# Performance work log

Hardware: AMD Instinct MI355X
Metric: run time of the kernel (lower is better)

## Reference

```python
import jax, jax.numpy as jnp
import numpy as np

DIM = 512
HEADS = 8
HEAD_DIM = DIM // HEADS
MLP_HIDDEN = int(DIM * 4.0)
B, N = 4, 2048
LS_INIT = 1e-5
EPS = 1e-5


def _layernorm(x, w, b):
    mu = jnp.mean(x, axis=-1, keepdims=True)
    var = jnp.mean(jnp.square(x - mu), axis=-1, keepdims=True)
    return (x - mu) * jax.lax.rsqrt(var + EPS) * w + b


def setup_inputs() -> dict:
    key = jax.random.key(0)
    ks = jax.random.split(key, 12)
    s = 0.02
    return {
        "x": jax.random.normal(ks[0], (B, N, DIM), jnp.float32),
        "rel_pos_bias": jax.random.normal(ks[1], (HEADS, N, N), jnp.float32),
        "qkv_w": jax.random.normal(ks[2], (DIM, 3 * DIM), jnp.float32) * s,
        "qkv_b": jnp.zeros((3 * DIM,), jnp.float32),
        "out_w": jax.random.normal(ks[3], (DIM, DIM), jnp.float32) * s,
        "out_b": jnp.zeros((DIM,), jnp.float32),
        "ln1_w": jnp.ones((DIM,), jnp.float32),
        "ln1_b": jnp.zeros((DIM,), jnp.float32),
        "ln2_w": jnp.ones((DIM,), jnp.float32),
        "ln2_b": jnp.zeros((DIM,), jnp.float32),
        "ffn_w1": jax.random.normal(ks[4], (DIM, MLP_HIDDEN), jnp.float32) * s,
        "ffn_b1": jnp.zeros((MLP_HIDDEN,), jnp.float32),
        "ffn_w2": jax.random.normal(ks[5], (MLP_HIDDEN, DIM), jnp.float32) * s,
        "ffn_b2": jnp.zeros((DIM,), jnp.float32),
        "gamma1": jnp.full((DIM,), LS_INIT, jnp.float32),
        "gamma2": jnp.full((DIM,), LS_INIT, jnp.float32),
    }


def reference(x, rel_pos_bias, qkv_w, qkv_b, out_w, out_b, ln1_w, ln1_b,
              ln2_w, ln2_b, ffn_w1, ffn_b1, ffn_w2, ffn_b2, gamma1, gamma2):
    # Pre-norm MHA with relative-position bias
    y = _layernorm(x, ln1_w, ln1_b)                       # [B,N,C]
    qkv = y @ qkv_w + qkv_b                               # [B,N,3C]
    qkv = qkv.reshape(B, N, 3, HEADS, HEAD_DIM)
    q = jnp.transpose(qkv[:, :, 0], (0, 2, 1, 3))         # [B,H,N,D]
    k = jnp.transpose(qkv[:, :, 1], (0, 2, 1, 3))
    v = jnp.transpose(qkv[:, :, 2], (0, 2, 1, 3))
    scale = 1.0 / np.sqrt(HEAD_DIM).astype(np.float32)
    attn = jnp.einsum("bhid,bhjd->bhij", q, k) * scale    # [B,H,N,N]
    attn = attn + rel_pos_bias[None]
    attn = jax.nn.softmax(attn, axis=-1)
    out = jnp.einsum("bhij,bhjd->bhid", attn, v)          # [B,H,N,D]
    out = jnp.transpose(out, (0, 2, 1, 3)).reshape(B, N, DIM)
    out = out @ out_w + out_b
    x = x + out * gamma1                                  # layer scale, no drop-path (eval)
    # FFN with exact GELU
    y2 = _layernorm(x, ln2_w, ln2_b)
    h = jax.nn.gelu(y2 @ ffn_w1 + ffn_b1, approximate=False)
    ffn_out = h @ ffn_w2 + ffn_b2
    x = x + ffn_out * gamma2
    return x
```

## Files before the change

### kernel.cpp

```cpp
#include <hip/hip_runtime.h>
#include <hip/hip_bf16.h>
#include <math.h>

#define SEQ 2048
#define BATCH 4
#define DM 512
#define NH 8
#define HD 64
#define HID 2048
#define ROWS (BATCH * SEQ)

typedef __attribute__((ext_vector_type(8))) short short8;
typedef __attribute__((ext_vector_type(4))) float f32x4;

__device__ __forceinline__ short f2bf(float f) {
    unsigned u = __float_as_uint(f);
    u += 0x7fff + ((u >> 16) & 1);
    return (short)(u >> 16);
}

__device__ __forceinline__ void gl2lds16(const void* g, void* l) {
    __builtin_amdgcn_global_load_lds(
        (const __attribute__((address_space(1))) void*)g,
        (__attribute__((address_space(3))) void*)l, 16, 0, 0);
}

__global__ __launch_bounds__(256) void tcast_all(
    const float* __restrict__ qkv_w, const float* __restrict__ out_w,
    const float* __restrict__ w1, const float* __restrict__ w2,
    short* __restrict__ o_qkv, short* __restrict__ o_out,
    short* __restrict__ o_w1, short* __restrict__ o_w2) {
    __shared__ float tile[32][33];
    int id = blockIdx.x;
    const float* W; short* O; int K, N;
    if (id < 768)       { W = qkv_w; O = o_qkv; K = 512;  N = 1536; }
    else if (id < 1024) { W = out_w; O = o_out; K = 512;  N = 512;  id -= 768; }
    else if (id < 2048) { W = w1;    O = o_w1;  K = 512;  N = 2048; id -= 1024; }
    else                { W = w2;    O = o_w2;  K = 2048; N = 512;  id -= 2048; }
    int tn = N / 32;
    int n0 = (id % tn) * 32, k0 = (id / tn) * 32;
    int tx = threadIdx.x, ty = threadIdx.y;
#pragma unroll
    for (int i = 0; i < 4; ++i)
        tile[ty + i * 8][tx] = W[(size_t)(k0 + ty + i * 8) * N + n0 + tx];
    __syncthreads();
#pragma unroll
    for (int i = 0; i < 4; ++i)
        O[(size_t)(n0 + ty + i * 8) * K + k0 + tx] = f2bf(tile[tx][ty + i * 8]);
}

__global__ __launch_bounds__(256) void ln_k(const float* __restrict__ X,
                                            const float* __restrict__ g,
                                            const float* __restrict__ bta,
                                            short* __restrict__ Y) {
    int t = threadIdx.x;
    int wv = t >> 6, ln = t & 63;
    size_t row = (size_t)blockIdx.x * 4 + wv;
    const float* xr = X + row * DM;
    float4 v0 = *(const float4*)(xr + ln * 4);
    float4 v1 = *(const float4*)(xr + 256 + ln * 4);
    float s = v0.x + v0.y + v0.z + v0.w + v1.x + v1.y + v1.z + v1.w;
    float q = v0.x * v0.x + v0.y * v0.y + v0.z * v0.z + v0.w * v0.w +
              v1.x * v1.x + v1.y * v1.y + v1.z * v1.z + v1.w * v1.w;
#pragma unroll
    for (int off = 1; off < 64; off <<= 1) {
        s += __shfl_xor(s, off);
        q += __shfl_xor(q, off);
    }
    float mean = s * (1.0f / 512.0f);
    float var = q * (1.0f / 512.0f) - mean * mean;
    float rstd = rsqrtf(var + 1e-5f);
    int c0 = ln * 4, c1 = 256 + ln * 4;
    ushort4 o0, o1;
    o0.x = (unsigned short)f2bf((v0.x - mean) * rstd * g[c0 + 0] + bta[c0 + 0]);
    o0.y = (unsigned short)f2bf((v0.y - mean) * rstd * g[c0 + 1] + bta[c0 + 1]);
    o0.z = (unsigned short)f2bf((v0.z - mean) * rstd * g[c0 + 2] + bta[c0 + 2]);
    o0.w = (unsigned short)f2bf((v0.w - mean) * rstd * g[c0 + 3] + bta[c0 + 3]);
    o1.x = (unsigned short)f2bf((v1.x - mean) * rstd * g[c1 + 0] + bta[c1 + 0]);
    o1.y = (unsigned short)f2bf((v1.y - mean) * rstd * g[c1 + 1] + bta[c1 + 1]);
    o1.z = (unsigned short)f2bf((v1.z - mean) * rstd * g[c1 + 2] + bta[c1 + 2]);
    o1.w = (unsigned short)f2bf((v1.w - mean) * rstd * g[c1 + 3] + bta[c1 + 3]);
    *(ushort4*)((unsigned short*)Y + row * DM + c0) = o0;
    *(ushort4*)((unsigned short*)Y + row * DM + c1) = o1;
}

template <int EPI, int TN>
__global__ __launch_bounds__(256) void gemm_bt(const short* __restrict__ A,
                                               const short* __restrict__ Bt,
                                               const float* __restrict__ bias,
                                               const float* __restrict__ gamma,
                                               const float* __restrict__ res,
                                               void* __restrict__ Cout,
                                               short* __restrict__ Cout2,
                                               int M, int N, int K) {
    constexpr int NI = TN / 32;
    __shared__ __attribute__((aligned(16))) short As0[128][32];
    __shared__ __attribute__((aligned(16))) short As1[128][32];
    __shared__ __attribute__((aligned(16))) short Bs0[TN][32];
    __shared__ __attribute__((aligned(16))) short Bs1[TN][32];
    int t = threadIdx.x;
    int w = t >> 6, ln = t & 63;
    int quad = ln >> 4, l15 = ln & 15;
    int n0 = blockIdx.x * TN, m0 = blockIdx.y * 128;
    int wm = (w & 1) * 64, wn = (w >> 1) * (TN / 2);

    int srow0 = w * 32 + (ln >> 2);
    int srow1 = srow0 + 16;
    int srowB = w * 16 + (ln >> 2);
    int schunk = (ln & 3) * 8;
    const short* Ag0 = A + (size_t)(m0 + srow0) * K + schunk;
    const short* Ag1 = A + (size_t)(m0 + srow1) * K + schunk;
    const short* Bg0 = Bt + (size_t)(n0 + srow0) * K + schunk;
    const short* Bg1 = Bt + (size_t)(n0 + srow1) * K + schunk;
    const short* BgB = Bt + (size_t)(n0 + srowB) * K + schunk;

    f32x4 acc[4][NI];
#pragma unroll
    for (int i = 0; i < 4; ++i)
#pragma unroll
        for (int j = 0; j < NI; ++j) acc[i][j] = (f32x4){0.f, 0.f, 0.f, 0.f};

    for (int k0 = 0; k0 < K; k0 += 64) {
        __syncthreads();
        gl2lds16(Ag0 + k0, &As0[srow0][schunk]);
        gl2lds16(Ag1 + k0, &As0[srow1][schunk]);
        gl2lds16(Ag0 + k0 + 32, &As1[srow0][schunk]);
        gl2lds16(Ag1 + k0 + 32, &As1[srow1][schunk]);
        if (TN == 128) {
            gl2lds16(Bg0 + k0, &Bs0[srow0 & (TN - 1)][schunk]);
            gl2lds16(Bg1 + k0, &Bs0[srow1 & (TN - 1)][schunk]);
            gl2lds16(Bg0 + k0 + 32, &Bs1[srow0 & (TN - 1)][schunk]);
            gl2lds16(Bg1 + k0 + 32, &Bs1[srow1 & (TN - 1)][schunk]);
        } else {
            gl2lds16(BgB + k0, &Bs0[srowB & (TN - 1)][schunk]);
            gl2lds16(BgB + k0 + 32, &Bs1[srowB & (TN - 1)][schunk]);
        }
        __syncthreads();
        {
            short8 af[4], bf[NI];
#pragma unroll
            for (int mi = 0; mi < 4; ++mi)
                af[mi] = *(const short8*)&As0[wm + mi * 16 + l15][quad * 8];
#pragma unroll
            for (int ni = 0; ni < NI; ++ni)
                bf[ni] = *(const short8*)&Bs0[wn + ni * 16 + l15][quad * 8];
#pragma unroll
            for (int mi = 0; mi < 4; ++mi)
#pragma unroll
                for (int ni = 0; ni < NI; ++ni)
                    acc[mi][ni] = __builtin_amdgcn_mfma_f32_16x16x32_bf16(
                        af[mi], bf[ni], acc[mi][ni], 0, 0, 0);
        }
        {
            short8 af[4], bf[NI];
#pragma unroll
            for (int mi = 0; mi < 4; ++mi)
                af[mi] = *(const short8*)&As1[wm + mi * 16 + l15][quad * 8];
#pragma unroll
            for (int ni = 0; ni < NI; ++ni)
                bf[ni] = *(const short8*)&Bs1[wn + ni * 16 + l15][quad * 8];
#pragma unroll
            for (int mi = 0; mi < 4; ++mi)
#pragma unroll
                for (int ni = 0; ni < NI; ++ni)
                    acc[mi][ni] = __builtin_amdgcn_mfma_f32_16x16x32_bf16(
                        af[mi], bf[ni], acc[mi][ni], 0, 0, 0);
        }
    }

    if (EPI == 3 && n0 >= 1024) {
#pragma unroll
        for (int mi = 0; mi < 4; ++mi) {
#pragma unroll
            for (int ni = 0; ni < NI; ++ni) {
                int col = n0 + wn + ni * 16 + l15;
                int d = col - 1024, hh = d >> 6, dd = d & 63;
                int row0 = m0 + wm + mi * 16 + quad * 4;
                int bb = row0 >> 11, key = row0 & 2047;
                float bs = bias[col];
                ushort4 pk;
                pk.x = (unsigned short)f2bf(acc[mi][ni][0] + bs);
                pk.y = (unsigned short)f2bf(acc[mi][ni][1] + bs);
                pk.z = (unsigned short)f2bf(acc[mi][ni][2] + bs);
                pk.w = (unsigned short)f2bf(acc[mi][ni][3] + bs);
                *(ushort4*)&Cout2[((size_t)(bb * 8 + hh) * 64 + dd) * 2048 + key] = pk;
            }
        }
    } else {
#pragma unroll
        for (int mi = 0; mi < 4; ++mi) {
#pragma unroll
            for (int ni = 0; ni < NI; ++ni) {
#pragma unroll
                for (int r = 0; r < 4; ++r) {
                    int row = m0 + wm + mi * 16 + quad * 4 + r;
                    int col = n0 + wn + ni * 16 + l15;
                    float v = acc[mi][ni][r] + bias[col];
                    if (EPI == 0) {
                        ((short*)Cout)[(size_t)row * N + col] = f2bf(v);
                    } else if (EPI == 1) {
                        float u = v * fmaf(v * v, 0.0713548162f, 1.59576912f);
                        float gg = v / (1.0f + __expf(-u));
                        ((short*)Cout)[(size_t)row * N + col] = f2bf(gg);
                    } else if (EPI == 2) {
                        ((float*)Cout)[(size_t)row * N + col] =
                            fmaf(v, gamma[col], res[(size_t)row * N + col]);
                    } else {
                        float sc = (n0 < 512) ? 0.18033688f : 1.0f;
                        ((short*)Cout)[(size_t)row * 1024 + col] = f2bf(v * sc);
                    }
                }
            }
        }
    }
}

__global__ __launch_bounds__(256, 4) void attn_k(const short* __restrict__ qkv,
                                                 const short* __restrict__ vT,
                                                 const float* __restrict__ bias,
                                                 float* __restrict__ O0,
                                                 float* __restrict__ O1,
                                                 float* __restrict__ lp) {
    __shared__ __attribute__((aligned(16))) short Ks[64 * 64];
    __shared__ __attribute__((aligned(16))) short Vs[64 * 64];
    __shared__ __attribute__((aligned(16))) short Ps[4][16 * 64];
    int t = threadIdx.x;
    int w = t >> 6, ln = t & 63, quad = ln >> 4, l15 = ln & 15;
    int idx = blockIdx.x;
    int half = idx >> 10;
    int rest = idx & 1023;
    int h = rest & 7, b = (rest >> 3) & 3, qt = rest >> 5;
    int qb = qt * 64 + w * 16;
    int jt0 = half * 16;
    int j0 = jt0 * 64;
    const size_t cbase = (size_t)b * SEQ * 1024;

    const short* qrow = qkv + cbase + (size_t)(qb + l15) * 1024 + h * 64;
    short8 qf0 = *(const short8*)(qrow + quad * 8);
    short8 qf1 = *(const short8*)(qrow + 32 + quad * 8);

    int kr = t >> 3, kc = t & 7;
    const short* kg = qkv + cbase + 512 + h * 64 + kc * 8;
    const short* vg = vT + ((size_t)(b * 8 + h) * 64) * 2048 + kc * 8;
    int kswz = ((kc ^ (kr & 7)) * 8);
    int kd0 = kr * 64 + kswz;
    int kd1 = kd0 + 32 * 64;

    const float* bias_q = bias + (size_t)h * SEQ * SEQ +
                          (size_t)(qb + l15) * SEQ + quad * 4;

    short8 ones;
#pragma unroll
    for (int i = 0; i < 8; ++i) ones[i] = (short)0x3F80;

    f32x4 o[4], ol;
#pragma unroll
    for (int db = 0; db < 4; ++db) o[db] = (f32x4){0.f, 0.f, 0.f, 0.f};
    ol = (f32x4){0.f, 0.f, 0.f, 0.f};

    int sw7 = l15 & 7;

    float4 pk0 = *(const float4*)(kg + (size_t)(j0 + kr) * 1024);
    float4 pk1 = *(const float4*)(kg + (size_t)(j0 + kr + 32) * 1024);
    float4 pv0 = *(const float4*)(vg + (size_t)kr * 2048 + j0);
    float4 pv1 = *(const float4*)(vg + (size_t)(kr + 32) * 2048 + j0);
    float4 bbc[4];
#pragma unroll
    for (int ni = 0; ni < 4; ++ni)
        bbc[ni] = *(const float4*)(bias_q + j0 + ni * 16);

    for (int jt = jt0; jt < jt0 + 16; ++jt) {
        __syncthreads();
        *(float4*)&Ks[kd0] = pk0;
        *(float4*)&Ks[kd1] = pk1;
        *(float4*)&Vs[kd0] = pv0;
        *(float4*)&Vs[kd1] = pv1;
        __syncthreads();
        int j1 = (jt < jt0 + 15) ? (jt + 1) * 64 : jt * 64;
        pk0 = *(const float4*)(kg + (size_t)(j1 + kr) * 1024);
        pk1 = *(const float4*)(kg + (size_t)(j1 + kr + 32) * 1024);
        pv0 = *(const float4*)(vg + (size_t)kr * 2048 + j1);
        pv1 = *(const float4*)(vg + (size_t)(kr + 32) * 2048 + j1);

        f32x4 s4[4];
#pragma unroll
        for (int ni = 0; ni < 4; ++ni) {
            short8 k0 = *(const short8*)&Ks[(ni * 16 + l15) * 64 + ((quad ^ sw7) * 8)];
            short8 k1 = *(const short8*)&Ks[(ni * 16 + l15) * 64 + (((4 + quad) ^ sw7) * 8)];
            s4[ni] = (f32x4){0.f, 0.f, 0.f, 0.f};
            s4[ni] = __builtin_amdgcn_mfma_f32_16x16x32_bf16(k0, qf0, s4[ni], 0, 0, 0);
            s4[ni] = __builtin_amdgcn_mfma_f32_16x16x32_bf16(k1, qf1, s4[ni], 0, 0, 0);
        }
#pragma unroll
        for (int ni = 0; ni < 4; ++ni) {
            float4 bb = bbc[ni];
            float2 plo, phi;
            plo.x = exp2f(fmaf(bb.x, 1.44269504f, s4[ni][0]));
            plo.y = exp2f(fmaf(bb.y, 1.44269504f, s4[ni][1]));
            phi.x = exp2f(fmaf(bb.z, 1.44269504f, s4[ni][2]));
            phi.y = exp2f(fmaf(bb.w, 1.44269504f, s4[ni][3]));
            bbc[ni] = *(const float4*)(bias_q + j1 + ni * 16);
            __hip_bfloat162 l2 = __float22bfloat162_rn(plo);
            __hip_bfloat162 h2 = __float22bfloat162_rn(phi);
            union { uint2 u; } pp;
            pp.u.x = *(unsigned*)&l2;
            pp.u.y = *(unsigned*)&h2;
            int c = ni * 2 + (quad >> 1);
            *(uint2*)&Ps[w][l15 * 64 + ((c ^ sw7) * 8) + (quad & 1) * 4] = pp.u;
        }
#pragma unroll
        for (int kk = 0; kk < 2; ++kk) {
            short8 ap = *(const short8*)&Ps[w][l15 * 64 + (((kk * 4 + quad) ^ sw7) * 8)];
#pragma unroll
            for (int db = 0; db < 4; ++db) {
                short8 vv = *(const short8*)&Vs[(db * 16 + l15) * 64 + (((kk * 4 + quad) ^ sw7) * 8)];
                o[db] = __builtin_amdgcn_mfma_f32_16x16x32_bf16(ap, vv, o[db], 0, 0, 0);
            }
            ol = __builtin_amdgcn_mfma_f32_16x16x32_bf16(ap, ones, ol, 0, 0, 0);
        }
    }
    float* Od = half ? O1 : O0;
    float* ld = lp + half * (32 * 2048);
#pragma unroll
    for (int r = 0; r < 4; ++r) {
        int qrow_g = b * SEQ + qb + quad * 4 + r;
#pragma unroll
        for (int db = 0; db < 4; ++db) {
            Od[(size_t)qrow_g * DM + h * 64 + db * 16 + l15] = o[db][r];
        }
        if (l15 == 0)
            ld[(size_t)(b * 8 + h) * 2048 + qb + quad * 4 + r] = ol[r];
    }
}

__global__ __launch_bounds__(256) void comb_k(const float* __restrict__ O0,
                                              const float* __restrict__ O1,
                                              const float* __restrict__ lp,
                                              short* __restrict__ Aout) {
    int t = threadIdx.x;
    int wv = t >> 6, ln = t & 63;
    size_t row = (size_t)blockIdx.x * 4 + wv;
    int b = (int)(row >> 11), q = (int)(row & 2047);
    int h = ln >> 3;
    float la = lp[(size_t)(b * 8 + h) * 2048 + q];
    float lb = lp[32 * 2048 + (size_t)(b * 8 + h) * 2048 + q];
    float inv = 1.0f / (la + lb);
    const float* p0 = O0 + row * DM + ln * 8;
    const float* p1 = O1 + row * DM + ln * 8;
    float4 a0 = *(const float4*)p0;
    float4 a1 = *(const float4*)(p0 + 4);
    float4 c0 = *(const float4*)p1;
    float4 c1 = *(const float4*)(p1 + 4);
    short8 o;
    o[0] = f2bf((a0.x + c0.x) * inv);
    o[1] = f2bf((a0.y + c0.y) * inv);
    o[2] = f2bf((a0.z + c0.z) * inv);
    o[3] = f2bf((a0.w + c0.w) * inv);
    o[4] = f2bf((a1.x + c1.x) * inv);
    o[5] = f2bf((a1.y + c1.y) * inv);
    o[6] = f2bf((a1.z + c1.z) * inv);
    o[7] = f2bf((a1.w + c1.w) * inv);
    *(short8*)(Aout + row * DM + ln * 8) = o;
}

extern "C" void kernel_launch(void* const* d_in, const int* in_sizes, int n_in,
                              void* d_out, int out_size, void* d_ws, size_t ws_size,
                              hipStream_t stream) {
    const float* x      = (const float*)d_in[0];
    const float* bias   = (const float*)d_in[1];
    const float* qkv_w  = (const float*)d_in[2];
    const float* qkv_b  = (const float*)d_in[3];
    const float* out_w  = (const float*)d_in[4];
    const float* out_b  = (const float*)d_in[5];
    const float* ln1_w  = (const float*)d_in[6];
    const float* ln1_b  = (const float*)d_in[7];
    const float* ln2_w  = (const float*)d_in[8];
    const float* ln2_b  = (const float*)d_in[9];
    const float* ffn_w1 = (const float*)d_in[10];
    const float* ffn_b1 = (const float*)d_in[11];
    const float* ffn_w2 = (const float*)d_in[12];
    const float* ffn_b2 = (const float*)d_in[13];
    const float* gamma1 = (const float*)d_in[14];
    const float* gamma2 = (const float*)d_in[15];
    float* out = (float*)d_out;

    short* wqkvT = (short*)d_ws;
    short* woutT = wqkvT + (size_t)1536 * 512;
    short* w1T   = woutT + (size_t)512 * 512;
    short* w2T   = w1T + (size_t)2048 * 512;
    short* y1    = w2T + (size_t)512 * 2048;
    short* qkvB  = y1 + (size_t)ROWS * DM;
    short* vTb   = qkvB + (size_t)ROWS * 1024;
    short* aoutB = vTb + (size_t)32 * 64 * 2048;
    float* x1    = (float*)(aoutB + (size_t)ROWS * DM);
    float* opart1 = x1 + (size_t)ROWS * DM;
    float* lpart  = opart1 + (size_t)ROWS * DM;
    float* opart0 = x1;
    short* hB    = qkvB;

    tcast_all<<<3072, dim3(32, 8), 0, stream>>>(qkv_w, out_w, ffn_w1, ffn_w2,
                                                wqkvT, woutT, w1T, w2T);
    ln_k<<<ROWS / 4, 256, 0, stream>>>(x, ln1_w, ln1_b, y1);
    gemm_bt<3, 128><<<dim3(1536 / 128, ROWS / 128), 256, 0, stream>>>(
        y1, wqkvT, qkv_b, nullptr, nullptr, qkvB, vTb, ROWS, 1536, 512);
    attn_k<<<2048, 256, 0, stream>>>(qkvB, vTb, bias, opart0, opart1, lpart);
    comb_k<<<ROWS / 4, 256, 0, stream>>>(opart0, opart1, lpart, aoutB);
    gemm_bt<2, 64><<<dim3(512 / 64, ROWS / 128), 256, 0, stream>>>(
        aoutB, woutT, out_b, gamma1, x, x1, nullptr, ROWS, 512, 512);
    ln_k<<<ROWS / 4, 256, 0, stream>>>(x1, ln2_w, ln2_b, y1);
    gemm_bt<1, 128><<<dim3(2048 / 128, ROWS / 128), 256, 0, stream>>>(
        y1, w1T, ffn_b1, nullptr, nullptr, hB, nullptr, ROWS, 2048, 512);
    gemm_bt<2, 64><<<dim3(512 / 64, ROWS / 128), 256, 0, stream>>>(
        hB, w2T, ffn_b2, gamma2, x1, out, nullptr, ROWS, 512, 2048);
}
```

Measured before the change: 446.0 us.

## Process two query groups per wave and double-buffer K/V via direct-to-LDS loads

Each attention block now covers 128 query rows instead of 64. Every wave computes two 16-row query groups against the same K/V tile, so each K/V fetch is reused twice and the grid is halved. K/V tiles are copied global-to-LDS asynchronously into double buffers, with the source column swizzled instead of the destination. This drops the register staging and one barrier per iteration. In exchange, register and LDS use per block go up, and launch bounds are lowered to 3 blocks per CU, which reduces occupancy.

```diff
diff --git a/kernel.cpp b/kernel.cpp
--- a/kernel.cpp
+++ b/kernel.cpp
@@ -215,121 +215,140 @@
     }
 }
 
-__global__ __launch_bounds__(256, 4) void attn_k(const short* __restrict__ qkv,
+__global__ __launch_bounds__(256, 3) void attn_k(const short* __restrict__ qkv,
                                                  const short* __restrict__ vT,
                                                  const float* __restrict__ bias,
                                                  float* __restrict__ O0,
                                                  float* __restrict__ O1,
                                                  float* __restrict__ lp) {
-    __shared__ __attribute__((aligned(16))) short Ks[64 * 64];
-    __shared__ __attribute__((aligned(16))) short Vs[64 * 64];
-    __shared__ __attribute__((aligned(16))) short Ps[4][16 * 64];
+    __shared__ __attribute__((aligned(16))) short Ks[2][64 * 64];
+    __shared__ __attribute__((aligned(16))) short Vs[2][64 * 64];
+    __shared__ __attribute__((aligned(16))) short Ps[4][2][16 * 64];
     int t = threadIdx.x;
     int w = t >> 6, ln = t & 63, quad = ln >> 4, l15 = ln & 15;
     int idx = blockIdx.x;
-    int half = idx >> 10;
-    int rest = idx & 1023;
+    int half = idx >> 9;
+    int rest = idx & 511;
     int h = rest & 7, b = (rest >> 3) & 3, qt = rest >> 5;
-    int qb = qt * 64 + w * 16;
+    int qb = qt * 128 + w * 16;
     int jt0 = half * 16;
     int j0 = jt0 * 64;
     const size_t cbase = (size_t)b * SEQ * 1024;
 
-    const short* qrow = qkv + cbase + (size_t)(qb + l15) * 1024 + h * 64;
-    short8 qf0 = *(const short8*)(qrow + quad * 8);
-    short8 qf1 = *(const short8*)(qrow + 32 + quad * 8);
+    const short* qrow0 = qkv + cbase + (size_t)(qb + l15) * 1024 + h * 64;
+    const short* qrow1 = qrow0 + (size_t)64 * 1024;
+    short8 qf[2][2];
+    qf[0][0] = *(const short8*)(qrow0 + quad * 8);
+    qf[0][1] = *(const short8*)(qrow0 + 32 + quad * 8);
+    qf[1][0] = *(const short8*)(qrow1 + quad * 8);
+    qf[1][1] = *(const short8*)(qrow1 + 32 + quad * 8);
 
     int kr = t >> 3, kc = t & 7;
-    const short* kg = qkv + cbase + 512 + h * 64 + kc * 8;
-    const short* vg = vT + ((size_t)(b * 8 + h) * 64) * 2048 + kc * 8;
-    int kswz = ((kc ^ (kr & 7)) * 8);
-    int kd0 = kr * 64 + kswz;
-    int kd1 = kd0 + 32 * 64;
-
-    const float* bias_q = bias + (size_t)h * SEQ * SEQ +
-                          (size_t)(qb + l15) * SEQ + quad * 4;
+    int sc = (kc ^ (kr & 7)) * 8;
+    const short* kgS = qkv + cbase + 512 + h * 64 + sc;
+    const short* vgS = vT + (size_t)(b * 8 + h) * 64 * 2048 + sc;
+
+    const float* bq0 = bias + (size_t)h * SEQ * SEQ +
+                       (size_t)(qb + l15) * SEQ + quad * 4;
+    const float* bq1 = bq0 + (size_t)64 * SEQ;
 
     short8 ones;
 #pragma unroll
     for (int i = 0; i < 8; ++i) ones[i] = (short)0x3F80;
 
-    f32x4 o[4], ol;
-#pragma unroll
-    for (int db = 0; db < 4; ++db) o[db] = (f32x4){0.f, 0.f, 0.f, 0.f};
-    ol = (f32x4){0.f, 0.f, 0.f, 0.f};
+    f32x4 o[2][4], ol[2];
+#pragma unroll
+    for (int qg = 0; qg < 2; ++qg) {
+#pragma unroll
+        for (int db = 0; db < 4; ++db) o[qg][db] = (f32x4){0.f, 0.f, 0.f, 0.f};
+        ol[qg] = (f32x4){0.f, 0.f, 0.f, 0.f};
+    }
 
     int sw7 = l15 & 7;
 
-    float4 pk0 = *(const float4*)(kg + (size_t)(j0 + kr) * 1024);
-    float4 pk1 = *(const float4*)(kg + (size_t)(j0 + kr + 32) * 1024);
-    float4 pv0 = *(const float4*)(vg + (size_t)kr * 2048 + j0);
-    float4 pv1 = *(const float4*)(vg + (size_t)(kr + 32) * 2048 + j0);
-    float4 bbc[4];
-#pragma unroll
-    for (int ni = 0; ni < 4; ++ni)
-        bbc[ni] = *(const float4*)(bias_q + j0 + ni * 16);
-
+    gl2lds16(kgS + (size_t)(j0 + kr) * 1024,      &Ks[0][t * 8]);
+    gl2lds16(kgS + (size_t)(j0 + 32 + kr) * 1024, &Ks[0][2048 + t * 8]);
+    gl2lds16(vgS + (size_t)kr * 2048 + j0,        &Vs[0][t * 8]);
+    gl2lds16(vgS + (size_t)(32 + kr) * 2048 + j0, &Vs[0][2048 + t * 8]);
+    float4 bbc[2][4];
+#pragma unroll
+    for (int ni = 0; ni < 4; ++ni) {
+        bbc[0][ni] = *(const float4*)(bq0 + j0 + ni * 16);
+        bbc[1][ni] = *(const float4*)(bq1 + j0 + ni * 16);
+    }
+
+    int cur = 0;
     for (int jt = jt0; jt < jt0 + 16; ++jt) {
         __syncthreads();
-        *(float4*)&Ks[kd0] = pk0;
-        *(float4*)&Ks[kd1] = pk1;
-        *(float4*)&Vs[kd0] = pv0;
-        *(float4*)&Vs[kd1] = pv1;
-        __syncthreads();
-        int j1 = (jt < jt0 + 15) ? (jt + 1) * 64 : jt * 64;
-        pk0 = *(const float4*)(kg + (size_t)(j1 + kr) * 1024);
-        pk1 = *(const float4*)(kg + (size_t)(j1 + kr + 32) * 1024);
-        pv0 = *(const float4*)(vg + (size_t)kr * 2048 + j1);
-        pv1 = *(const float4*)(vg + (size_t)(kr + 32) * 2048 + j1);
-
-        f32x4 s4[4];
+        int j1 = (jt < jt0 + 15) ? (jt + 1) * 64 : j0;
+        int nxt = cur ^ 1;
+        gl2lds16(kgS + (size_t)(j1 + kr) * 1024,      &Ks[nxt][t * 8]);
+        gl2lds16(kgS + (size_t)(j1 + 32 + kr) * 1024, &Ks[nxt][2048 + t * 8]);
+        gl2lds16(vgS + (size_t)kr * 2048 + j1,        &Vs[nxt][t * 8]);
+        gl2lds16(vgS + (size_t)(32 + kr) * 2048 + j1, &Vs[nxt][2048 + t * 8]);
+
+        f32x4 s4[2][4];
 #pragma unroll
         for (int ni = 0; ni < 4; ++ni) {
-            short8 k0 = *(const short8*)&Ks[(ni * 16 + l15) * 64 + ((quad ^ sw7) * 8)];
-            short8 k1 = *(const short8*)&Ks[(ni * 16 + l15) * 64 + (((4 + quad) ^ sw7) * 8)];
-            s4[ni] = (f32x4){0.f, 0.f, 0.f, 0.f};
-            s4[ni] = __builtin_amdgcn_mfma_f32_16x16x32_bf16(k0, qf0, s4[ni], 0, 0, 0);
-            s4[ni] = __builtin_amdgcn_mfma_f32_16x16x32_bf16(k1, qf1, s4[ni], 0, 0, 0);
-        }
-#pragma unroll
-        for (int ni = 0; ni < 4; ++ni) {
-            float4 bb = bbc[ni];
-            float2 plo, phi;
-            plo.x = exp2f(fmaf(bb.x, 1.44269504f, s4[ni][0]));
-            plo.y = exp2f(fmaf(bb.y, 1.44269504f, s4[ni][1]));
-            phi.x = exp2f(fmaf(bb.z, 1.44269504f, s4[ni][2]));
-            phi.y = exp2f(fmaf(bb.w, 1.44269504f, s4[ni][3]));
-            bbc[ni] = *(const float4*)(bias_q + j1 + ni * 16);
-            __hip_bfloat162 l2 = __float22bfloat162_rn(plo);
-            __hip_bfloat162 h2 = __float22bfloat162_rn(phi);
-            union { uint2 u; } pp;
-            pp.u.x = *(unsigned*)&l2;
-            pp.u.y = *(unsigned*)&h2;
-            int c = ni * 2 + (quad >> 1);
-            *(uint2*)&Ps[w][l15 * 64 + ((c ^ sw7) * 8) + (quad & 1) * 4] = pp.u;
+            short8 k0 = *(const short8*)&Ks[cur][(ni * 16 + l15) * 64 + ((quad ^ sw7) * 8)];
+            short8 k1 = *(const short8*)&Ks[cur][(ni * 16 + l15) * 64 + (((4 + quad) ^ sw7) * 8)];
+#pragma unroll
+            for (int qg = 0; qg < 2; ++qg) {
+                f32x4 z = (f32x4){0.f, 0.f, 0.f, 0.f};
+                z = __builtin_amdgcn_mfma_f32_16x16x32_bf16(k0, qf[qg][0], z, 0, 0, 0);
+                s4[qg][ni] = __builtin_amdgcn_mfma_f32_16x16x32_bf16(k1, qf[qg][1], z, 0, 0, 0);
+            }
+        }
+#pragma unroll
+        for (int qg = 0; qg < 2; ++qg) {
+#pragma unroll
+            for (int ni = 0; ni < 4; ++ni) {
+                float4 bb = bbc[qg][ni];
+                float2 plo, phi;
+                plo.x = exp2f(fmaf(bb.x, 1.44269504f, s4[qg][ni][0]));
+                plo.y = exp2f(fmaf(bb.y, 1.44269504f, s4[qg][ni][1]));
+                phi.x = exp2f(fmaf(bb.z, 1.44269504f, s4[qg][ni][2]));
+                phi.y = exp2f(fmaf(bb.w, 1.44269504f, s4[qg][ni][3]));
+                bbc[qg][ni] = *(const float4*)((qg ? bq1 : bq0) + j1 + ni * 16);
+                __hip_bfloat162 l2 = __float22bfloat162_rn(plo);
+                __hip_bfloat162 h2 = __float22bfloat162_rn(phi);
+                union { uint2 u; } pp;
+                pp.u.x = *(unsigned*)&l2;
+                pp.u.y = *(unsigned*)&h2;
+                int c = ni * 2 + (quad >> 1);
+                *(uint2*)&Ps[w][qg][l15 * 64 + ((c ^ sw7) * 8) + (quad & 1) * 4] = pp.u;
+            }
         }
 #pragma unroll
         for (int kk = 0; kk < 2; ++kk) {
-            short8 ap = *(const short8*)&Ps[w][l15 * 64 + (((kk * 4 + quad) ^ sw7) * 8)];
+            short8 ap0 = *(const short8*)&Ps[w][0][l15 * 64 + (((kk * 4 + quad) ^ sw7) * 8)];
+            short8 ap1 = *(const short8*)&Ps[w][1][l15 * 64 + (((kk * 4 + quad) ^ sw7) * 8)];
 #pragma unroll
             for (int db = 0; db < 4; ++db) {
-                short8 vv = *(const short8*)&Vs[(db * 16 + l15) * 64 + (((kk * 4 + quad) ^ sw7) * 8)];
-                o[db] = __builtin_amdgcn_mfma_f32_16x16x32_bf16(ap, vv, o[db], 0, 0, 0);
-            }
-            ol = __builtin_amdgcn_mfma_f32_16x16x32_bf16(ap, ones, ol, 0, 0, 0);
-        }
+                short8 vv = *(const short8*)&Vs[cur][(db * 16 + l15) * 64 + (((kk * 4 + quad) ^ sw7) * 8)];
+                o[0][db] = __builtin_amdgcn_mfma_f32_16x16x32_bf16(ap0, vv, o[0][db], 0, 0, 0);
+                o[1][db] = __builtin_amdgcn_mfma_f32_16x16x32_bf16(ap1, vv, o[1][db], 0, 0, 0);
+            }
+            ol[0] = __builtin_amdgcn_mfma_f32_16x16x32_bf16(ap0, ones, ol[0], 0, 0, 0);
+            ol[1] = __builtin_amdgcn_mfma_f32_16x16x32_bf16(ap1, ones, ol[1], 0, 0, 0);
+        }
+        cur = nxt;
     }
     float* Od = half ? O1 : O0;
     float* ld = lp + half * (32 * 2048);
 #pragma unroll
-    for (int r = 0; r < 4; ++r) {
-        int qrow_g = b * SEQ + qb + quad * 4 + r;
-#pragma unroll
-        for (int db = 0; db < 4; ++db) {
-            Od[(size_t)qrow_g * DM + h * 64 + db * 16 + l15] = o[db][r];
-        }
-        if (l15 == 0)
-            ld[(size_t)(b * 8 + h) * 2048 + qb + quad * 4 + r] = ol[r];
+    for (int qg = 0; qg < 2; ++qg) {
+#pragma unroll
+        for (int r = 0; r < 4; ++r) {
+            int qloc = qb + qg * 64 + quad * 4 + r;
+            int qrow_g = b * SEQ + qloc;
+#pragma unroll
+            for (int db = 0; db < 4; ++db) {
+                Od[(size_t)qrow_g * DM + h * 64 + db * 16 + l15] = o[qg][db][r];
+            }
+            if (l15 == 0)
+                ld[(size_t)(b * 8 + h) * 2048 + qloc] = ol[qg][r];
+        }
     }
 }
 
@@ -403,7 +422,7 @@
     ln_k<<<ROWS / 4, 256, 0, stream>>>(x, ln1_w, ln1_b, y1);
     gemm_bt<3, 128><<<dim3(1536 / 128, ROWS / 128), 256, 0, stream>>>(
         y1, wqkvT, qkv_b, nullptr, nullptr, qkvB, vTb, ROWS, 1536, 512);
-    attn_k<<<2048, 256, 0, stream>>>(qkvB, vTb, bias, opart0, opart1, lpart);
+    attn_k<<<1024, 256, 0, stream>>>(qkvB, vTb, bias, opart0, opart1, lpart);
     comb_k<<<ROWS / 4, 256, 0, stream>>>(opart0, opart1, lpart, aoutB);
     gemm_bt<2, 64><<<dim3(512 / 64, ROWS / 128), 256, 0, stream>>>(
         aoutB, woutT, out_b, gamma1, x, x1, nullptr, ROWS, 512, 512);
```

New measurement: 438.5 us. No clear change (-1.7%).
